# Optimization experiments

Measured on AMD Instinct MI355X. Metric: run time of the kernel, lower is better.

The kernel has to match this reference:

```python
import jax, jax.numpy as jnp
import numpy as np
import math

B, S, E, H = 4, 2048, 1024, 16
D = E // H
INFINITY = 1000000.0

def setup_inputs() -> dict:
    key = jax.random.key(0)
    ks = jax.random.split(key, 10)
    std = 1.0 / math.sqrt(E)
    inp = {
        "x": jax.random.normal(ks[0], (B, S, E), dtype=jnp.float32),
        "mask": jax.random.randint(ks[1], (B, S), 0, 2).astype(jnp.bool_),
        "WQ_w": jax.random.uniform(ks[2], (E, E), jnp.float32, -std, std),
        "WQ_b": jax.random.uniform(ks[3], (E,), jnp.float32, -std, std),
        "WK_w": jax.random.uniform(ks[4], (E, E), jnp.float32, -std, std),
        "WK_b": jax.random.uniform(ks[5], (E,), jnp.float32, -std, std),
        "WV_w": jax.random.uniform(ks[6], (E, E), jnp.float32, -std, std),
        "WV_b": jax.random.uniform(ks[7], (E,), jnp.float32, -std, std),
        "WO_w": jax.random.uniform(ks[8], (E, E), jnp.float32, -std, std),
        "WO_b": jax.random.uniform(ks[9], (E,), jnp.float32, -std, std),
    }
    return inp

def reference(x, mask, WQ_w, WQ_b, WK_w, WK_b, WV_w, WV_b, WO_w, WO_b):
    # Linear layers: y = x @ W.T + b (torch convention)
    q = (x @ WQ_w.T + WQ_b).reshape(B, S, H, D).transpose(0, 2, 1, 3)  # (B,H,S,D)
    k = (x @ WK_w.T + WK_b).reshape(B, S, H, D).transpose(0, 2, 1, 3)
    v = (x @ WV_w.T + WV_b).reshape(B, S, H, D).transpose(0, 2, 1, 3)
    score = jnp.einsum("bhqd,bhkd->bhqk", q, k) / math.sqrt(D)  # (B,H,S,S)
    # additive key mask: -infinity where mask is False
    inv_mask = (~mask).astype(jnp.float32)[:, None, None, :]  # (B,1,1,S)
    score = score - inv_mask * INFINITY
    attn = jax.nn.softmax(score, axis=-1)
    o = jnp.einsum("bhqk,bhkd->bhqd", attn, v)  # (B,H,S,D)
    o = o.transpose(0, 2, 1, 3).reshape(B, S, E)
    o = o @ WO_w.T + WO_b
    o = jnp.abs(o * mask.astype(jnp.float32)[:, :, None])
    return o
```

## Files before the change

### kernel.cpp

```cpp
#include <hip/hip_runtime.h>
#include <math.h>

#define B_ 4
#define S_ 2048
#define E_ 1024
#define H_ 16
#define D_ 64
#define MTOT (B_*S_)

typedef _Float16 half8v __attribute__((ext_vector_type(8)));
typedef _Float16 half4v __attribute__((ext_vector_type(4)));
typedef float f32x4 __attribute__((ext_vector_type(4)));
typedef float f32x16 __attribute__((ext_vector_type(16)));
typedef unsigned uint4v __attribute__((ext_vector_type(4)));

typedef __attribute__((address_space(1))) const void gconst_void;
typedef __attribute__((address_space(3))) void lds_void;

#define MFMA16(a,b,c) __builtin_amdgcn_mfma_f32_16x16x32_f16((a),(b),(c),0,0,0)
#define MFMA32(a,b,c) __builtin_amdgcn_mfma_f32_32x32x16_f16((a),(b),(c),0,0,0)

#define QSCALE 0.18033688011112042f

static __device__ __forceinline__ unsigned cvt_pk_u32(float a, float b) {
  return __builtin_bit_cast(unsigned, __builtin_amdgcn_cvt_pkrtz(a, b));
}

#if __has_builtin(__builtin_amdgcn_permlane32_swap)
static __device__ __forceinline__ void pl32_swap(unsigned a, unsigned b,
                                                 unsigned& rlo, unsigned& rhi) {
  auto r = __builtin_amdgcn_permlane32_swap(a, b, false, false);
  rlo = r[0]; rhi = r[1];
}
#else
static __device__ __forceinline__ void pl32_swap(unsigned a, unsigned b,
                                                 unsigned& rlo, unsigned& rhi) {
  const int hi = (threadIdx.x & 63) >> 5;
  unsigned t = __shfl_xor(hi ? a : b, 32);
  rlo = hi ? t : a;
  rhi = hi ? b : t;
}
#endif

static __device__ __forceinline__ float partner32(float v, int hi) {
  unsigned u = __builtin_bit_cast(unsigned, v);
  unsigned lo_, hi_;
  pl32_swap(u, u, lo_, hi_);
  return __builtin_bit_cast(float, hi ? lo_ : hi_);
}

__global__ __launch_bounds__(256) void cvt_w4(const float* __restrict__ w0, const float* __restrict__ w1,
                                              const float* __restrict__ w2, const float* __restrict__ w3,
                                              _Float16* __restrict__ o0, _Float16* __restrict__ o1,
                                              _Float16* __restrict__ o2, _Float16* __restrict__ o3) {
  const int z = blockIdx.y;
  const float* in = (z == 0) ? w0 : (z == 1) ? w1 : (z == 2) ? w2 : w3;
  _Float16* out = (z == 0) ? o0 : (z == 1) ? o1 : (z == 2) ? o2 : o3;
  int i = (blockIdx.x * 256 + threadIdx.x) * 4;
  float4 v = *(const float4*)(in + i);
  half4v o;
  o[0] = (_Float16)v.x; o[1] = (_Float16)v.y; o[2] = (_Float16)v.z; o[3] = (_Float16)v.w;
  *(half4v*)(out + i) = o;
}

__global__ __launch_bounds__(256) void zero_out(float* __restrict__ out) {
  const size_t i = ((size_t)blockIdx.x * 256 + threadIdx.x) * 4;
  float4 z = make_float4(0.f, 0.f, 0.f, 0.f);
  *(float4*)(out + i) = z;
}

__global__ __launch_bounds__(256) void mask_prep(const unsigned char* __restrict__ mraw,
                                                 _Float16* __restrict__ maskc,
                                                 float* __restrict__ qmask,
                                                 int* __restrict__ ks,
                                                 int* __restrict__ nkpa) {
  __shared__ int flags[2];
  __shared__ int psum[256];
  const int b = blockIdx.x, tid = threadIdx.x;
  if (tid < 2) flags[tid] = 1;
  __syncthreads();
  const unsigned int* w = (const unsigned int*)mraw;
  for (int i = tid; i < 2048; i += 256) {
    unsigned int v = w[i];
    if (!(v == 0u || v == 1u)) flags[0] = 0;
    if (!(v == 0u || v == 0x3f800000u)) flags[1] = 0;
  }
  __syncthreads();
  const int is_i32 = flags[0], is_f32 = flags[1];
  int m[8]; int cnt = 0;
  for (int i = 0; i < 8; ++i) {
    const int idx = b * 2048 + tid * 8 + i;
    int mv;
    if (is_i32)      mv = ((const int*)mraw)[idx];
    else if (is_f32) mv = (((const unsigned int*)mraw)[idx] != 0u);
    else             mv = (mraw[idx] != 0);
    m[i] = mv; cnt += mv;
    qmask[idx] = mv ? 1.0f : 0.0f;
  }
  psum[tid] = cnt;
  __syncthreads();
  for (int off = 1; off < 256; off <<= 1) {
    int u = (tid >= off) ? psum[tid - off] : 0;
    __syncthreads();
    psum[tid] += u;
    __syncthreads();
  }
  const int total = psum[255];
  int base = psum[tid] - cnt;
  for (int i = 0; i < 8; ++i)
    if (m[i]) ks[b * 2048 + (base++)] = tid * 8 + i;
  for (int j = tid; j < 2048; j += 256)
    maskc[b * 2048 + j] = (j < total) ? (_Float16)0.0f : (_Float16)(-60000.0f);
  __syncthreads();
  const int lastv = (total > 0) ? ks[b * 2048 + total - 1] : 0;
  for (int j = total + tid; j < 2048; j += 256)
    ks[b * 2048 + j] = lastv;
  if (tid == 0) nkpa[b] = (total + 127) & ~127;
}

__global__ __launch_bounds__(256) void cvt_xc(const float* __restrict__ x,
                                              const int* __restrict__ ks,
                                              const int* __restrict__ nkpa,
                                              _Float16* __restrict__ xc) {
  const int b = blockIdx.y, j = blockIdx.x;
  if (j >= nkpa[b]) return;
  const int s = ks[b * 2048 + j];
  const float* src = x + (size_t)(b * 2048 + s) * E_;
  _Float16* dst = xc + (size_t)(b * 2048 + j) * E_;
  const int i = threadIdx.x * 4;
  float4 v = *(const float4*)(src + i);
  half4v o;
  o[0] = (_Float16)v.x; o[1] = (_Float16)v.y; o[2] = (_Float16)v.z; o[3] = (_Float16)v.w;
  *(half4v*)(dst + i) = o;
}

__device__ __forceinline__ void stage128x32(const _Float16* __restrict__ g, int ld,
                                            _Float16* lds, int wid, int lane) {
#pragma unroll
  for (int j = 0; j < 2; ++j) {
    const int c = j * 256 + wid * 64 + lane;
    const _Float16* src = g + (size_t)(c >> 2) * ld + (c & 3) * 8;
    _Float16* dst = lds + (size_t)(j * 256 + wid * 64) * 8;
    __builtin_amdgcn_global_load_lds((gconst_void*)src, (lds_void*)dst, 16, 0, 0);
  }
}

__device__ __forceinline__ void stage64x32(const _Float16* __restrict__ g, int ld,
                                           _Float16* lds, int wid, int lane) {
  const int c = wid * 64 + lane;
  const _Float16* src = g + (size_t)(c >> 2) * ld + (c & 3) * 8;
  _Float16* dst = lds + (size_t)(wid * 64) * 8;
  __builtin_amdgcn_global_load_lds((gconst_void*)src, (lds_void*)dst, 16, 0, 0);
}

__global__ __launch_bounds__(256) void qkv_gemm(
    const _Float16* __restrict__ xc, const int* __restrict__ nkpa,
    const _Float16* __restrict__ wq, const _Float16* __restrict__ wk, const _Float16* __restrict__ wv,
    const float* __restrict__ bq, const float* __restrict__ bkp, const float* __restrict__ bvp,
    _Float16* __restrict__ Qc, _Float16* __restrict__ Kc, _Float16* __restrict__ Vc) {
  const int id = blockIdx.x;
  const int m = id / 48;
  const int r = id % 48;
  const int by = r / 3, z = r % 3;
  const int bb = m >> 4, tt = m & 15;
  if (tt * 128 >= nkpa[bb]) return;
  __shared__ _Float16 As[128 * 32];
  __shared__ _Float16 Bs[64 * 32];
  const int tid = threadIdx.x, lane = tid & 63, wid = tid >> 6;
  const int g = lane >> 4, r16 = lane & 15;
  const int bm = m * 128, bn = by * 64;
  const _Float16* w = (z == 0) ? wq : (z == 1) ? wk : wv;
  const float* bias = (z == 0) ? bq : (z == 1) ? bkp : bvp;
  const int wr = wid >> 1, wc = wid & 1;
  f32x4 acc[4][2] = {};
  for (int k0 = 0; k0 < E_; k0 += 32) {
    stage128x32(xc + (size_t)bm * E_ + k0, E_, As, wid, lane);
    stage64x32(w + (size_t)bn * E_ + k0, E_, Bs, wid, lane);
    __syncthreads();
    half8v a[4], bf[2];
#pragma unroll
    for (int i = 0; i < 4; ++i) a[i] = *(const half8v*)&As[(wr * 64 + i * 16 + r16) * 32 + g * 8];
#pragma unroll
    for (int j = 0; j < 2; ++j) bf[j] = *(const half8v*)&Bs[(wc * 32 + j * 16 + r16) * 32 + g * 8];
#pragma unroll
    for (int i = 0; i < 4; ++i)
#pragma unroll
      for (int j = 0; j < 2; ++j) acc[i][j] = MFMA16(a[i], bf[j], acc[i][j]);
    __syncthreads();
  }
#pragma unroll
  for (int i = 0; i < 4; ++i) {
#pragma unroll
    for (int j = 0; j < 2; ++j) {
      const int gn = bn + wc * 32 + j * 16 + r16;
      const float bb2 = bias[gn];
      const int h = gn >> 6, d = gn & 63;
      const int gm0 = bm + wr * 64 + i * 16 + g * 4;
      const int b_ = gm0 >> 11, s0 = gm0 & (S_ - 1);
      const size_t bhbase = (size_t)(b_ * H_ + h) * S_ * D_;
      if (z == 2) {
        half4v v4;
#pragma unroll
        for (int ii = 0; ii < 4; ++ii) v4[ii] = (_Float16)(acc[i][j][ii] + bb2);
        *(half4v*)&Vc[bhbase + (size_t)(s0 >> 4) * (D_ * 16) + d * 16 + (s0 & 15)] = v4;
      } else if (z == 1) {
#pragma unroll
        for (int ii = 0; ii < 4; ++ii) {
          const int s = s0 + ii;
          Kc[bhbase + (size_t)(s >> 5) * 2048 + (d >> 4) * 512 + (s & 31) * 16 + (d & 15)] =
              (_Float16)(acc[i][j][ii] + bb2);
        }
      } else {
#pragma unroll
        for (int ii = 0; ii < 4; ++ii)
          Qc[bhbase + (size_t)(s0 + ii) * D_ + d] = (_Float16)((acc[i][j][ii] + bb2) * QSCALE);
      }
    }
  }
}

__global__ __launch_bounds__(512) void attn_kernel(
    const _Float16* __restrict__ Qc, const _Float16* __restrict__ Kc, const _Float16* __restrict__ Vc,
    const _Float16* __restrict__ maskc, const int* __restrict__ nkpa,
    _Float16* __restrict__ Oc) {
  __shared__ float mlds[4][64][36];
  _Float16* smask = (_Float16*)&mlds[0][0][0];
  const int tid = threadIdx.x, lane = tid & 63, wid = tid >> 6;
  const int c = lane & 31, hi = lane >> 5;
  const int qg = wid & 3, kh = wid >> 2;
  const int id = blockIdx.x;
  const int slot = id & 7, hbh = (id >> 3) & 7, t = id >> 6;
  const int hb = hbh * 8 + slot;
  const int b = hb >> 4, h = hb & 15;
  const int nkp = nkpa[b];
  if (t * 128 >= nkp) return;
  const size_t bh = (size_t)(b * H_ + h);
  const _Float16* Qb = Qc + bh * S_ * D_;
  const _Float16* Kb = Kc + bh * S_ * D_;
  const _Float16* Vb = Vc + bh * S_ * D_;

  *((half4v*)smask + tid) = *((const half4v*)(maskc + (size_t)b * S_) + tid);

  const int jq = t * 128 + qg * 32 + c;

  half8v qb[4];
#pragma unroll
  for (int kc = 0; kc < 4; ++kc)
    qb[kc] = *(const half8v*)&Qb[(size_t)jq * D_ + 16 * kc + 8 * hi];

  half8v bone = {};
  if (hi == 0) bone[0] = (_Float16)1.0f;
  const f32x16 fzero = {};

  f32x16 oacc[2] = {};
  float mrun = -1e30f, lrun = 0.f;
  const int laneoff = c * 16 + 8 * hi;
  const int nkh = nkp >> 1;
  const int kb0 = kh * nkh;

  __syncthreads();

  half8v kaf[4];
  {
    const _Float16* ktb = Kb + (size_t)(kb0 >> 5) * 2048 + laneoff;
#pragma unroll
    for (int kc = 0; kc < 4; ++kc) kaf[kc] = *(const half8v*)&ktb[kc * 512];
  }
  _Float16 mv = smask[kb0 + c];

  for (int kb = kb0; kb < kb0 + nkh; kb += 32) {
    half8v amask = {};
    if (hi == 0) amask[0] = mv;
    __builtin_amdgcn_s_setprio(1);
    f32x16 sc = MFMA32(amask, bone, fzero);
    sc = MFMA32(kaf[0], qb[0], sc);
    sc = MFMA32(kaf[1], qb[1], sc);
    sc = MFMA32(kaf[2], qb[2], sc);
    sc = MFMA32(kaf[3], qb[3], sc);
    __builtin_amdgcn_s_setprio(0);
    const int kbn = (kb + 32 < kb0 + nkh) ? kb + 32 : kb0;
    {
      const _Float16* ktb = Kb + (size_t)(kbn >> 5) * 2048 + laneoff;
#pragma unroll
      for (int kc = 0; kc < 4; ++kc) kaf[kc] = *(const half8v*)&ktb[kc * 512];
    }
    mv = smask[kbn + c];
    const _Float16* v_base = Vb + (size_t)(kb >> 4) * (D_ * 16) + laneoff;
    half8v va00 = *(const half8v*)&v_base[0];
    half8v va01 = *(const half8v*)&v_base[512];
    half8v va10 = *(const half8v*)&v_base[1024];
    half8v va11 = *(const half8v*)&v_base[1024 + 512];
    float t0 = fmaxf(sc[0], sc[4]), t1 = fmaxf(sc[1], sc[5]);
    float t2 = fmaxf(sc[2], sc[6]), t3 = fmaxf(sc[3], sc[7]);
    t0 = fmaxf(fmaxf(sc[8], sc[12]), t0);
    t1 = fmaxf(fmaxf(sc[9], sc[13]), t1);
    t2 = fmaxf(fmaxf(sc[10], sc[14]), t2);
    t3 = fmaxf(fmaxf(sc[11], sc[15]), t3);
    float pmax = fmaxf(fmaxf(t0, t1), fmaxf(t2, t3));
    pmax = fmaxf(pmax, partner32(pmax, hi));
    if (__any(pmax > mrun + 11.0f)) {
      float mnew = fmaxf(mrun, pmax);
      float corr = __builtin_amdgcn_exp2f(mrun - mnew);
      mrun = mnew;
      lrun *= corr;
#pragma unroll
      for (int dt = 0; dt < 2; ++dt)
#pragma unroll
        for (int r = 0; r < 16; ++r) oacc[dt][r] *= corr;
    }
    float ps0 = 0.f, ps1 = 0.f;
#pragma unroll
    for (int sl = 0; sl < 2; ++sl) {
      const int bs = 8 * sl;
      float p0 = __builtin_amdgcn_exp2f(sc[bs + 0] - mrun);
      float p1 = __builtin_amdgcn_exp2f(sc[bs + 1] - mrun);
      float p2 = __builtin_amdgcn_exp2f(sc[bs + 2] - mrun);
      float p3 = __builtin_amdgcn_exp2f(sc[bs + 3] - mrun);
      float p4 = __builtin_amdgcn_exp2f(sc[bs + 4] - mrun);
      float p5 = __builtin_amdgcn_exp2f(sc[bs + 5] - mrun);
      float p6 = __builtin_amdgcn_exp2f(sc[bs + 6] - mrun);
      float p7 = __builtin_amdgcn_exp2f(sc[bs + 7] - mrun);
      ps0 += (p0 + p1) + (p2 + p3);
      ps1 += (p4 + p5) + (p6 + p7);
      unsigned uA = cvt_pk_u32(p0, p1);
      unsigned uB = cvt_pk_u32(p2, p3);
      unsigned uC = cvt_pk_u32(p4, p5);
      unsigned uD = cvt_pk_u32(p6, p7);
      unsigned w0, w1, w2, w3;
      pl32_swap(uA, uC, w0, w2);
      pl32_swap(uB, uD, w1, w3);
      uint4v u4 = {w0, w1, w2, w3};
      half8v pb = __builtin_bit_cast(half8v, u4);
      __builtin_amdgcn_s_setprio(1);
      oacc[0] = MFMA32(sl ? va10 : va00, pb, oacc[0]);
      oacc[1] = MFMA32(sl ? va11 : va01, pb, oacc[1]);
      __builtin_amdgcn_s_setprio(0);
    }
    lrun += ps0 + ps1;
  }
  lrun += partner32(lrun, hi);
  __syncthreads();
  if (kh == 1) {
    float* p = &mlds[qg][lane][0];
#pragma unroll
    for (int dt = 0; dt < 2; ++dt)
#pragma unroll
      for (int rr = 0; rr < 4; ++rr) {
        float4 v4 = make_float4(oacc[dt][4 * rr], oacc[dt][4 * rr + 1],
                                oacc[dt][4 * rr + 2], oacc[dt][4 * rr + 3]);
        *(float4*)&p[dt * 16 + rr * 4] = v4;
      }
    p[32] = mrun;
    p[33] = lrun;
  }
  __syncthreads();
  if (kh == 0) {
    const float* p = &mlds[qg][lane][0];
    const float mB = p[32], lB = p[33];
    const float mS = fmaxf(mrun, mB);
    const float cA = __builtin_amdgcn_exp2f(mrun - mS);
    const float cB = __builtin_amdgcn_exp2f(mB - mS);
    const float inv = 1.0f / (lrun * cA + lB * cB);
    const float fA = cA * inv, fB = cB * inv;
    _Float16* orow = Oc + ((size_t)(b * S_ + jq)) * E_ + h * D_;
#pragma unroll
    for (int dt = 0; dt < 2; ++dt)
#pragma unroll
      for (int rr = 0; rr < 4; ++rr) {
        float4 vB = *(const float4*)&p[dt * 16 + rr * 4];
        half4v o4;
        o4[0] = (_Float16)(oacc[dt][4 * rr + 0] * fA + vB.x * fB);
        o4[1] = (_Float16)(oacc[dt][4 * rr + 1] * fA + vB.y * fB);
        o4[2] = (_Float16)(oacc[dt][4 * rr + 2] * fA + vB.z * fB);
        o4[3] = (_Float16)(oacc[dt][4 * rr + 3] * fA + vB.w * fB);
        *(half4v*)&orow[32 * dt + 8 * rr + 4 * hi] = o4;
      }
  }
}

__global__ __launch_bounds__(256) void oproj_gemm(
    const _Float16* __restrict__ Oc, const _Float16* __restrict__ wo, const float* __restrict__ bo,
    const int* __restrict__ ks, const int* __restrict__ nkpa, float* __restrict__ out) {
  const int id = blockIdx.x;
  const int jt = id / 32;
  const int rem = id % 32;
  const int bb = rem / 8, by = rem % 8;
  if (jt * 64 >= nkpa[bb]) return;
  __shared__ _Float16 As[64 * 32];
  __shared__ _Float16 Bs[128 * 32];
  const int tid = threadIdx.x, lane = tid & 63, wid = tid >> 6;
  const int g = lane >> 4, r16 = lane & 15;
  const int bm = bb * 2048 + jt * 64, bn = by * 128;
  const int wr = wid >> 1, wc = wid & 1;
  f32x4 acc[2][4] = {};
  for (int k0 = 0; k0 < E_; k0 += 32) {
    stage64x32(Oc + (size_t)bm * E_ + k0, E_, As, wid, lane);
    stage128x32(wo + (size_t)bn * E_ + k0, E_, Bs, wid, lane);
    __syncthreads();
    half8v a[2], bf[4];
#pragma unroll
    for (int i = 0; i < 2; ++i) a[i] = *(const half8v*)&As[(wr * 32 + i * 16 + r16) * 32 + g * 8];
#pragma unroll
    for (int j = 0; j < 4; ++j) bf[j] = *(const half8v*)&Bs[(wc * 64 + j * 16 + r16) * 32 + g * 8];
#pragma unroll
    for (int i = 0; i < 2; ++i)
#pragma unroll
      for (int j = 0; j < 4; ++j) acc[i][j] = MFMA16(a[i], bf[j], acc[i][j]);
    __syncthreads();
  }
#pragma unroll
  for (int i = 0; i < 2; ++i) {
#pragma unroll
    for (int j = 0; j < 4; ++j) {
      const int gn = bn + wc * 64 + j * 16 + r16;
      const float bb2 = bo[gn];
      const int gm0 = bm + wr * 32 + i * 16 + g * 4;
#pragma unroll
      for (int ii = 0; ii < 4; ++ii) {
        const int gm = gm0 + ii;
        const int b_ = gm >> 11, j_ = gm & (S_ - 1);
        const int sorig = ks[b_ * 2048 + j_];
        const float y = acc[i][j][ii] + bb2;
        out[((size_t)(b_ * S_ + sorig)) * E_ + gn] = fabsf(y);
      }
    }
  }
}

extern "C" void kernel_launch(void* const* d_in, const int* in_sizes, int n_in,
                              void* d_out, int out_size, void* d_ws, size_t ws_size,
                              hipStream_t stream) {
  const float* x = (const float*)d_in[0];
  const unsigned char* mask = (const unsigned char*)d_in[1];
  const float* WQ_w = (const float*)d_in[2];
  const float* WQ_b = (const float*)d_in[3];
  const float* WK_w = (const float*)d_in[4];
  const float* WK_b = (const float*)d_in[5];
  const float* WV_w = (const float*)d_in[6];
  const float* WV_b = (const float*)d_in[7];
  const float* WO_w = (const float*)d_in[8];
  const float* WO_b = (const float*)d_in[9];

  char* ws = (char*)d_ws;
  size_t off = 0;
  _Float16* xc  = (_Float16*)(ws + off); off += (size_t)MTOT * E_ * 2;
  _Float16* wqh = (_Float16*)(ws + off); off += (size_t)E_ * E_ * 2;
  _Float16* wkh = (_Float16*)(ws + off); off += (size_t)E_ * E_ * 2;
  _Float16* wvh = (_Float16*)(ws + off); off += (size_t)E_ * E_ * 2;
  _Float16* woh = (_Float16*)(ws + off); off += (size_t)E_ * E_ * 2;
  _Float16* Qc  = (_Float16*)(ws + off); off += (size_t)MTOT * E_ * 2;
  _Float16* Kc  = (_Float16*)(ws + off); off += (size_t)MTOT * E_ * 2;
  _Float16* Vc  = (_Float16*)(ws + off); off += (size_t)MTOT * E_ * 2;
  _Float16* Oc  = (_Float16*)(ws + off); off += (size_t)MTOT * E_ * 2;
  _Float16* maskcf = (_Float16*)(ws + off); off += (size_t)B_ * S_ * 2;
  float* qmaskf = (float*)(ws + off); off += (size_t)B_ * S_ * 4;
  int* ksl      = (int*)(ws + off); off += (size_t)B_ * S_ * 4;
  int* nkpa     = (int*)(ws + off); off += 64;
  if (ws_size < off) return;

  const int NW = E_ * E_;
  mask_prep<<<dim3(B_), dim3(256), 0, stream>>>(mask, maskcf, qmaskf, ksl, nkpa);
  cvt_w4<<<dim3(NW / 4 / 256, 4), dim3(256), 0, stream>>>(WQ_w, WK_w, WV_w, WO_w,
                                                          wqh, wkh, wvh, woh);
  cvt_xc<<<dim3(S_, B_), dim3(256), 0, stream>>>(x, ksl, nkpa, xc);
  zero_out<<<dim3(MTOT * E_ / 4 / 256), dim3(256), 0, stream>>>((float*)d_out);
  qkv_gemm<<<dim3(64 * 48), dim3(256), 0, stream>>>(
      xc, nkpa, wqh, wkh, wvh, WQ_b, WK_b, WV_b, Qc, Kc, Vc);
  attn_kernel<<<dim3((S_ / 128) * H_ * B_), dim3(512), 0, stream>>>(
      Qc, Kc, Vc, maskcf, nkpa, Oc);
  oproj_gemm<<<dim3(32 * 32), dim3(256), 0, stream>>>(Oc, woh, WO_b, ksl, nkpa, (float*)d_out);
}
```

Before: 144.9 us.

## Fuse Q, K, V projections into one block sharing the staged x tile

Each qkv_gemm block now computes Q, K and V for the same 128x64 output tile. It stages the x tile once and the three weight tiles into separate LDS buffers, then issues MFMAs for all three accumulators. This cuts redundant x loads and reduces the grid from 3072 to 1024 blocks, with tiles ordered row-tile-major across batches. The cost is three times the accumulator registers and more LDS per block, which may lower occupancy.

```diff
diff --git a/kernel.cpp b/kernel.cpp
--- a/kernel.cpp
+++ b/kernel.cpp
@@ -159,33 +159,47 @@
     const float* __restrict__ bq, const float* __restrict__ bkp, const float* __restrict__ bvp,
     _Float16* __restrict__ Qc, _Float16* __restrict__ Kc, _Float16* __restrict__ Vc) {
   const int id = blockIdx.x;
-  const int m = id / 48;
-  const int r = id % 48;
-  const int by = r / 3, z = r % 3;
-  const int bb = m >> 4, tt = m & 15;
+  const int tt = id / 64;
+  const int rem = id % 64;
+  const int bb = rem / 16, by = rem % 16;
   if (tt * 128 >= nkpa[bb]) return;
+  const int m = bb * 16 + tt;
   __shared__ _Float16 As[128 * 32];
-  __shared__ _Float16 Bs[64 * 32];
+  __shared__ _Float16 BsQ[64 * 32];
+  __shared__ _Float16 BsK[64 * 32];
+  __shared__ _Float16 BsV[64 * 32];
   const int tid = threadIdx.x, lane = tid & 63, wid = tid >> 6;
   const int g = lane >> 4, r16 = lane & 15;
   const int bm = m * 128, bn = by * 64;
-  const _Float16* w = (z == 0) ? wq : (z == 1) ? wk : wv;
-  const float* bias = (z == 0) ? bq : (z == 1) ? bkp : bvp;
   const int wr = wid >> 1, wc = wid & 1;
-  f32x4 acc[4][2] = {};
+  f32x4 accQ[4][2] = {}, accK[4][2] = {}, accV[4][2] = {};
   for (int k0 = 0; k0 < E_; k0 += 32) {
     stage128x32(xc + (size_t)bm * E_ + k0, E_, As, wid, lane);
-    stage64x32(w + (size_t)bn * E_ + k0, E_, Bs, wid, lane);
+    stage64x32(wq + (size_t)bn * E_ + k0, E_, BsQ, wid, lane);
+    stage64x32(wk + (size_t)bn * E_ + k0, E_, BsK, wid, lane);
+    stage64x32(wv + (size_t)bn * E_ + k0, E_, BsV, wid, lane);
     __syncthreads();
     half8v a[4], bf[2];
 #pragma unroll
     for (int i = 0; i < 4; ++i) a[i] = *(const half8v*)&As[(wr * 64 + i * 16 + r16) * 32 + g * 8];
 #pragma unroll
-    for (int j = 0; j < 2; ++j) bf[j] = *(const half8v*)&Bs[(wc * 32 + j * 16 + r16) * 32 + g * 8];
+    for (int j = 0; j < 2; ++j) bf[j] = *(const half8v*)&BsQ[(wc * 32 + j * 16 + r16) * 32 + g * 8];
 #pragma unroll
     for (int i = 0; i < 4; ++i)
 #pragma unroll
-      for (int j = 0; j < 2; ++j) acc[i][j] = MFMA16(a[i], bf[j], acc[i][j]);
+      for (int j = 0; j < 2; ++j) accQ[i][j] = MFMA16(a[i], bf[j], accQ[i][j]);
+#pragma unroll
+    for (int j = 0; j < 2; ++j) bf[j] = *(const half8v*)&BsK[(wc * 32 + j * 16 + r16) * 32 + g * 8];
+#pragma unroll
+    for (int i = 0; i < 4; ++i)
+#pragma unroll
+      for (int j = 0; j < 2; ++j) accK[i][j] = MFMA16(a[i], bf[j], accK[i][j]);
+#pragma unroll
+    for (int j = 0; j < 2; ++j) bf[j] = *(const half8v*)&BsV[(wc * 32 + j * 16 + r16) * 32 + g * 8];
+#pragma unroll
+    for (int i = 0; i < 4; ++i)
+#pragma unroll
+      for (int j = 0; j < 2; ++j) accV[i][j] = MFMA16(a[i], bf[j], accV[i][j]);
     __syncthreads();
   }
 #pragma unroll
@@ -193,27 +207,31 @@
 #pragma unroll
     for (int j = 0; j < 2; ++j) {
       const int gn = bn + wc * 32 + j * 16 + r16;
-      const float bb2 = bias[gn];
       const int h = gn >> 6, d = gn & 63;
       const int gm0 = bm + wr * 64 + i * 16 + g * 4;
       const int b_ = gm0 >> 11, s0 = gm0 & (S_ - 1);
       const size_t bhbase = (size_t)(b_ * H_ + h) * S_ * D_;
-      if (z == 2) {
-        half4v v4;
-#pragma unroll
-        for (int ii = 0; ii < 4; ++ii) v4[ii] = (_Float16)(acc[i][j][ii] + bb2);
-        *(half4v*)&Vc[bhbase + (size_t)(s0 >> 4) * (D_ * 16) + d * 16 + (s0 & 15)] = v4;
-      } else if (z == 1) {
+      {
+        const float bbq = bq[gn];
+#pragma unroll
+        for (int ii = 0; ii < 4; ++ii)
+          Qc[bhbase + (size_t)(s0 + ii) * D_ + d] = (_Float16)((accQ[i][j][ii] + bbq) * QSCALE);
+      }
+      {
+        const float bbk = bkp[gn];
 #pragma unroll
         for (int ii = 0; ii < 4; ++ii) {
           const int s = s0 + ii;
           Kc[bhbase + (size_t)(s >> 5) * 2048 + (d >> 4) * 512 + (s & 31) * 16 + (d & 15)] =
-              (_Float16)(acc[i][j][ii] + bb2);
+              (_Float16)(accK[i][j][ii] + bbk);
         }
-      } else {
-#pragma unroll
-        for (int ii = 0; ii < 4; ++ii)
-          Qc[bhbase + (size_t)(s0 + ii) * D_ + d] = (_Float16)((acc[i][j][ii] + bb2) * QSCALE);
+      }
+      {
+        const float bbv = bvp[gn];
+        half4v v4;
+#pragma unroll
+        for (int ii = 0; ii < 4; ++ii) v4[ii] = (_Float16)(accV[i][j][ii] + bbv);
+        *(half4v*)&Vc[bhbase + (size_t)(s0 >> 4) * (D_ * 16) + d * 16 + (s0 & 15)] = v4;
       }
     }
   }
@@ -464,7 +482,7 @@
                                                           wqh, wkh, wvh, woh);
   cvt_xc<<<dim3(S_, B_), dim3(256), 0, stream>>>(x, ksl, nkpa, xc);
   zero_out<<<dim3(MTOT * E_ / 4 / 256), dim3(256), 0, stream>>>((float*)d_out);
-  qkv_gemm<<<dim3(64 * 48), dim3(256), 0, stream>>>(
+  qkv_gemm<<<dim3(1024), dim3(256), 0, stream>>>(
       xc, nkpa, wqh, wkh, wvh, WQ_b, WK_b, WV_b, Qc, Kc, Vc);
   attn_kernel<<<dim3((S_ / 128) * H_ * B_), dim3(512), 0, stream>>>(
       Qc, Kc, Vc, maskcf, nkpa, Oc);
```

Measured after the change: 186.0 us. 28.3% more time.
